# Performance work log

Measured on AMD Instinct MI355X. Metric: run time of the kernel, lower is better.

## Reference

```python
import jax, jax.numpy as jnp
import numpy as np

B, S, D, E, TOP_K = 2, 1024, 1024, 8, 2
H = 4 * D  # FFN hidden


def setup_inputs() -> dict:
    key = jax.random.key(0)
    ks = jax.random.split(key, 12)
    sc = 0.02
    return {
        "x": jax.random.normal(ks[0], (B, S, D), jnp.float32),
        # gate: nn.Linear(D, E) -> weight [E, D], bias [E]; routing bias param [E]
        "Wg": jax.random.normal(ks[1], (E, D), jnp.float32) * sc,
        "bg": jnp.zeros((E,), jnp.float32),
        "bias": jnp.zeros((E,), jnp.float32),
        # routed experts: stacked Linear(D,4D) and Linear(4D,D) weights (torch layout [out,in])
        "W1": jax.random.normal(ks[2], (E, H, D), jnp.float32) * sc,
        "b1": jnp.zeros((E, H), jnp.float32),
        "W2": jax.random.normal(ks[3], (E, D, H), jnp.float32) * sc,
        "b2": jnp.zeros((E, D), jnp.float32),
        # shared expert
        "Ws1": jax.random.normal(ks[4], (H, D), jnp.float32) * sc,
        "bs1": jnp.zeros((H,), jnp.float32),
        "Ws2": jax.random.normal(ks[5], (D, H), jnp.float32) * sc,
        "bs2": jnp.zeros((D,), jnp.float32),
    }


def reference(x, Wg, bg, bias, W1, b1, W2, b2, Ws1, bs1, Ws2, bs2):
    b, s, d = x.shape
    xf = x.reshape(-1, d)  # [T, D]
    T = xf.shape[0]

    # sigmoid gating with learnable routing bias
    scores = jax.nn.sigmoid(xf @ Wg.T + bg + bias)          # [T, E]
    top_scores, top_idx = jax.lax.top_k(scores, TOP_K)      # [T, K]

    # per-token per-expert combine weights (zero for unselected experts)
    weights = jnp.zeros((T, E), scores.dtype)
    weights = weights.at[jnp.arange(T)[:, None], top_idx].add(top_scores)  # [T, E]

    # dense grouped expert MLP (mask-and-matmul form of gather-GEMM-scatter)
    h = jax.nn.gelu(jnp.einsum("td,ehd->teh", xf, W1) + b1, approximate=False)  # [T, E, H]
    eo = jnp.einsum("teh,edh->ted", h, W2) + b2                                  # [T, E, D]
    combined = jnp.einsum("ted,te->td", eo, weights)                             # [T, D]

    # shared expert applied to every token
    shared = jax.nn.gelu(xf @ Ws1.T + bs1, approximate=False) @ Ws2.T + bs2      # [T, D]

    return (shared + combined).reshape(b, s, d)
```

## Files before the change

kernel.cpp:

```cpp
#include <hip/hip_runtime.h>
#include <hip/hip_bf16.h>
#include <math.h>

#define NTOK 2048
#define DDIM 1024
#define HDIM 4096
#define NEXP 8
#define NROWS (3 * NTOK)
#define KSPLIT2 2

typedef __bf16 bf16x8 __attribute__((ext_vector_type(8)));
typedef float f32x4 __attribute__((ext_vector_type(4)));
typedef __attribute__((address_space(1))) char as1_char;
typedef __attribute__((address_space(3))) char as3_char;

__device__ __forceinline__ void async16(const void* g, void* l) {
  __builtin_amdgcn_global_load_lds((as1_char*)g, (as3_char*)l, 16, 0, 0);
}

__device__ __forceinline__ float gelu_fast(float v) {
  const float x = v * 0.70710678118654752f;
  const float ax = fabsf(x);
  const float t = __builtin_amdgcn_rcpf(1.0f + 0.3275911f * ax);
  float p = 1.061405429f;
  p = p * t - 1.453152027f;
  p = p * t + 1.421413741f;
  p = p * t - 0.284496736f;
  p = p * t + 0.254829592f;
  const float y = 1.0f - p * t * __expf(-ax * ax);
  const float erfv = copysignf(y, x);
  return 0.5f * v * (1.0f + erfv);
}

__device__ __forceinline__ int off_of(const int* __restrict__ counts, int e) {
  if (e >= NEXP) return 2 * NTOK;
  int s = 0;
  for (int i = 0; i < e; ++i) s += counts[i];
  return s;
}

__device__ __forceinline__ void cvt2048(const float* __restrict__ src,
                                        __hip_bfloat16* __restrict__ dst,
                                        int tid) {
  const size_t i = (size_t)tid * 8;
  const float4 a = *(const float4*)(src + i);
  const float4 b = *(const float4*)(src + i + 4);
  union { __hip_bfloat16 h[8]; uint4 u; } p;
  p.h[0] = __float2bfloat16(a.x); p.h[1] = __float2bfloat16(a.y);
  p.h[2] = __float2bfloat16(a.z); p.h[3] = __float2bfloat16(a.w);
  p.h[4] = __float2bfloat16(b.x); p.h[5] = __float2bfloat16(b.y);
  p.h[6] = __float2bfloat16(b.z); p.h[7] = __float2bfloat16(b.w);
  *(uint4*)(dst + i) = p.u;
}

__global__ void __launch_bounds__(256) moe_pre(
    const float* __restrict__ x, const float* __restrict__ Wg,
    const float* __restrict__ bg, const float* __restrict__ bias,
    const float* __restrict__ W1, const float* __restrict__ Ws1,
    __hip_bfloat16* __restrict__ xbf, __hip_bfloat16* __restrict__ W1bf,
    __hip_bfloat16* __restrict__ Ws1bf, float* __restrict__ out,
    int* __restrict__ counts, int* __restrict__ topk_idx,
    float* __restrict__ topk_w, int* __restrict__ slot) {
  const int b = blockIdx.x, tid = threadIdx.x;
  if (b < 512) {
    const int t = b * 4 + (tid >> 6);
    const int lane = tid & 63;
    float xv[16];
#pragma unroll
    for (int q = 0; q < 16; ++q) xv[q] = x[(size_t)t * DDIM + q * 64 + lane];
    float sc[NEXP];
#pragma unroll
    for (int e = 0; e < NEXP; ++e) {
      float s = 0.f;
#pragma unroll
      for (int q = 0; q < 16; ++q) s += xv[q] * Wg[(size_t)e * DDIM + q * 64 + lane];
#pragma unroll
      for (int o = 32; o > 0; o >>= 1) s += __shfl_xor(s, o, 64);
      sc[e] = 1.0f / (1.0f + expf(-(s + bg[e] + bias[e])));
    }
    if (lane == 0) {
      int k0 = 0;
      for (int e = 1; e < NEXP; ++e)
        if (sc[e] > sc[k0]) k0 = e;
      int k1 = (k0 == 0) ? 1 : 0;
      for (int e = 0; e < NEXP; ++e) {
        if (e == k0) continue;
        if (sc[e] > sc[k1]) k1 = e;
      }
      topk_idx[t * 2 + 0] = k0;
      topk_idx[t * 2 + 1] = k1;
      topk_w[t * 2 + 0] = sc[k0];
      topk_w[t * 2 + 1] = sc[k1];
      slot[t * 2 + 0] = atomicAdd(&counts[k0], 1);
      slot[t * 2 + 1] = atomicAdd(&counts[k1], 1);
    }
    return;
  }
  const int cb = b - 512;
  if (cb < 1024) { cvt2048(x + (size_t)cb * 2048, xbf + (size_t)cb * 2048, tid); return; }
  if (cb < 17408) { const size_t o = (size_t)(cb - 1024) * 2048; cvt2048(W1 + o, W1bf + o, tid); return; }
  if (cb < 19456) { const size_t o = (size_t)(cb - 17408) * 2048; cvt2048(Ws1 + o, Ws1bf + o, tid); return; }
  const size_t o = (size_t)(cb - 19456) * 2048 + (size_t)tid * 8;
  *(float4*)(out + o) = make_float4(0.f, 0.f, 0.f, 0.f);
  *(float4*)(out + o + 4) = make_float4(0.f, 0.f, 0.f, 0.f);
}

__device__ __forceinline__ void gemm_core(const char* const ga[4], const char* const gb[4],
                                          char* sm, int Kbytes, int tid,
                                          f32x4 acc[4][4]) {
  const int w = tid >> 6, l = tid & 63;
  const int lr = l & 15, quad = l >> 4;
  const int wr = w >> 1, wc = w & 1;
  const int s8 = lr & 7;
  const int slot0 = (quad ^ s8) * 16;
  const int slot1 = ((4 + quad) ^ s8) * 16;
  const int abase = (wr * 64 + lr) * 128;
  const int bbase = 16384 + (wc * 64 + lr) * 128;
  const int niter = Kbytes >> 7;

  auto stage = [&](int it, int buf) {
    char* base = sm + buf * 32768;
    const int kb = it * 128;
#pragma unroll
    for (int q = 0; q < 4; ++q) {
      async16(ga[q] + kb, base + w * 4096 + q * 1024);
      async16(gb[q] + kb, base + 16384 + w * 4096 + q * 1024);
    }
  };

  stage(0, 0);
  for (int i = 0; i < niter; ++i) {
    const int cur = i & 1;
    if (i + 1 < niter) {
      stage(i + 1, cur ^ 1);
      __builtin_amdgcn_s_waitcnt(0x0F78);
    } else {
      __builtin_amdgcn_s_waitcnt(0x0F70);
    }
    __builtin_amdgcn_s_barrier();
    const char* rb = sm + cur * 32768;
    bf16x8 av[4][2], bv[4][2];
#pragma unroll
    for (int i2 = 0; i2 < 4; ++i2) {
      av[i2][0] = *(const bf16x8*)(rb + abase + i2 * 2048 + slot0);
      av[i2][1] = *(const bf16x8*)(rb + abase + i2 * 2048 + slot1);
    }
#pragma unroll
    for (int j = 0; j < 4; ++j) {
      bv[j][0] = *(const bf16x8*)(rb + bbase + j * 2048 + slot0);
      bv[j][1] = *(const bf16x8*)(rb + bbase + j * 2048 + slot1);
    }
#pragma unroll
    for (int s = 0; s < 2; ++s)
#pragma unroll
      for (int i2 = 0; i2 < 4; ++i2)
#pragma unroll
        for (int j = 0; j < 4; ++j)
          acc[i2][j] = __builtin_amdgcn_mfma_f32_16x16x32_bf16(av[i2][s], bv[j][s], acc[i2][j], 0, 0, 0);
    __builtin_amdgcn_s_barrier();
  }
}

__device__ __forceinline__ void gemm2_core(const char* const ga[4], const char* const gb[2],
                                           char* sm, int Kbytes, int tid,
                                           f32x4 acc[4][2]) {
  const int w = tid >> 6, l = tid & 63;
  const int lr = l & 15, quad = l >> 4;
  const int wr = w >> 1, wc = w & 1;
  const int s8 = lr & 7;
  const int slot0 = (quad ^ s8) * 16;
  const int slot1 = ((4 + quad) ^ s8) * 16;
  const int abase = (wr * 64 + lr) * 128;
  const int bbase = 16384 + (wc * 32 + lr) * 128;
  const int niter = Kbytes >> 7;

  auto stage = [&](int it, int buf) {
    char* base = sm + buf * 24576;
    const int kb = it * 128;
#pragma unroll
    for (int q = 0; q < 4; ++q)
      async16(ga[q] + kb, base + w * 4096 + q * 1024);
#pragma unroll
    for (int q = 0; q < 2; ++q)
      async16(gb[q] + kb, base + 16384 + w * 2048 + q * 1024);
  };

  stage(0, 0);
  for (int i = 0; i < niter; ++i) {
    const int cur = i & 1;
    if (i + 1 < niter) {
      stage(i + 1, cur ^ 1);
      __builtin_amdgcn_s_waitcnt(0x0F76);
    } else {
      __builtin_amdgcn_s_waitcnt(0x0F70);
    }
    __builtin_amdgcn_s_barrier();
    const char* rb = sm + cur * 24576;
    bf16x8 av[4][2], bv[2][2];
#pragma unroll
    for (int i2 = 0; i2 < 4; ++i2) {
      av[i2][0] = *(const bf16x8*)(rb + abase + i2 * 2048 + slot0);
      av[i2][1] = *(const bf16x8*)(rb + abase + i2 * 2048 + slot1);
    }
#pragma unroll
    for (int j = 0; j < 2; ++j) {
      bv[j][0] = *(const bf16x8*)(rb + bbase + j * 2048 + slot0);
      bv[j][1] = *(const bf16x8*)(rb + bbase + j * 2048 + slot1);
    }
#pragma unroll
    for (int s = 0; s < 2; ++s)
#pragma unroll
      for (int i2 = 0; i2 < 4; ++i2)
#pragma unroll
        for (int j = 0; j < 2; ++j)
          acc[i2][j] = __builtin_amdgcn_mfma_f32_16x16x32_bf16(av[i2][s], bv[j][s], acc[i2][j], 0, 0, 0);
    __builtin_amdgcn_s_barrier();
  }
}

__device__ __forceinline__ void xcd_decode(int hw, int& g, int& m) {
  m = (hw >> 3) & 7;
  g = (hw & 7) + 8 * (hw >> 6);
}

__global__ void moe_scatter(const int* __restrict__ counts,
                            const int* __restrict__ topk_idx, const float* __restrict__ topk_w,
                            const int* __restrict__ slot,
                            int* __restrict__ row_token, float* __restrict__ row_w) {
  const int t = blockIdx.x * blockDim.x + threadIdx.x;
  if (t >= NTOK) return;
#pragma unroll
  for (int k = 0; k < 2; ++k) {
    const int e = topk_idx[t * 2 + k];
    const int rg = off_of(counts, e) + slot[t * 2 + k];
    row_token[rg] = t;
    row_w[rg] = topk_w[t * 2 + k];
  }
  row_token[2 * NTOK + t] = t;
  row_w[2 * NTOK + t] = 1.0f;
}

__device__ __forceinline__ void cvt_w2_quota(int b, const float* __restrict__ W2,
                                             const float* __restrict__ Ws2,
                                             __hip_bfloat16* __restrict__ W2bf,
                                             __hip_bfloat16* __restrict__ Ws2bf,
                                             int tid) {
  const float* src;
  __hip_bfloat16* dst;
  size_t base;
  if (b < 4096) { src = W2; dst = W2bf; base = (size_t)b * 8192; }
  else          { src = Ws2; dst = Ws2bf; base = (size_t)(b - 4096) * 8192; }
#pragma unroll
  for (int k = 0; k < 8; ++k) {
    const size_t i = base + (size_t)k * 1024 + (size_t)tid * 4;
    const float4 a = *(const float4*)(src + i);
    union { __hip_bfloat16 h[4]; uint2 u; } p;
    p.h[0] = __float2bfloat16(a.x); p.h[1] = __float2bfloat16(a.y);
    p.h[2] = __float2bfloat16(a.z); p.h[3] = __float2bfloat16(a.w);
    *(uint2*)(dst + i) = p.u;
  }
}

__global__ void __launch_bounds__(256) moe_gemm1(
    const __hip_bfloat16* __restrict__ xbf, const __hip_bfloat16* __restrict__ W1bf,
    const float* __restrict__ b1, const __hip_bfloat16* __restrict__ Ws1bf,
    const float* __restrict__ bs1, const int* __restrict__ counts,
    const int* __restrict__ row_token,
    __hip_bfloat16* __restrict__ h1, const float* __restrict__ W2,
    const float* __restrict__ Ws2, __hip_bfloat16* __restrict__ W2bf,
    __hip_bfloat16* __restrict__ Ws2bf) {
  __shared__ alignas(16) char sm[65536];
  const int tid = threadIdx.x;
  int g, m;
  xcd_decode(blockIdx.x, g, m);
  const int nt = m + 8 * (g & 3);
  const int mt = (g >> 2) & 15;
  const int e = g >> 6;
  const int cnt = (e < NEXP) ? counts[e] : NTOK;
  if (mt * 128 >= cnt) {
    cvt_w2_quota(blockIdx.x, W2, Ws2, W2bf, Ws2bf, tid);
    return;
  }
  const int off = off_of(counts, e);
  const __hip_bfloat16* Bw = (e < NEXP) ? (W1bf + (size_t)e * HDIM * DDIM) : Ws1bf;
  const float* bb = (e < NEXP) ? (b1 + e * HDIM) : bs1;

  const int w = tid >> 6, l = tid & 63;
  const int rl8 = l >> 3;
  const int cg = ((l & 7) ^ rl8) * 16;

  const char* ga[4];
  const char* gb[4];
#pragma unroll
  for (int q = 0; q < 4; ++q) {
    const int r = mt * 128 + w * 32 + q * 8 + rl8;
    const int c = (r < cnt) ? r : (cnt - 1);
    const int tok = row_token[off + c];
    ga[q] = (const char*)xbf + (size_t)tok * (DDIM * 2) + cg;
    gb[q] = (const char*)Bw + (size_t)(nt * 128 + w * 32 + q * 8 + rl8) * (DDIM * 2) + cg;
  }

  f32x4 acc[4][4] = {};
  gemm_core(ga, gb, sm, DDIM * 2, tid, acc);

  const int lr = l & 15, quad = l >> 4, wr = w >> 1, wc = w & 1;
#pragma unroll
  for (int i = 0; i < 4; ++i) {
#pragma unroll
    for (int r = 0; r < 4; ++r) {
      const int rowe = mt * 128 + wr * 64 + i * 16 + quad * 4 + r;
      if (rowe >= cnt) continue;
      const size_t orow = (size_t)(off + rowe) * HDIM;
#pragma unroll
      for (int j = 0; j < 4; ++j) {
        const int h = nt * 128 + wc * 64 + j * 16 + lr;
        const float v = acc[i][j][r] + bb[h];
        h1[orow + h] = __float2bfloat16(gelu_fast(v));
      }
    }
  }
  cvt_w2_quota(blockIdx.x, W2, Ws2, W2bf, Ws2bf, tid);
}

__global__ void __launch_bounds__(256) moe_gemm2(
    const __hip_bfloat16* __restrict__ h1, const __hip_bfloat16* __restrict__ W2bf,
    const float* __restrict__ b2, const __hip_bfloat16* __restrict__ Ws2bf,
    const float* __restrict__ bs2, const int* __restrict__ counts,
    const int* __restrict__ row_token,
    const float* __restrict__ row_w, float* __restrict__ out) {
  __shared__ alignas(16) char sm[49152];
  int g, m;
  xcd_decode(blockIdx.x, g, m);
  const int nt = m + 8 * (g & 1);
  const int kc = (g >> 1) & 1;
  const int mt = (g >> 2) & 15;
  const int e = g >> 6;
  const int cnt = (e < NEXP) ? counts[e] : NTOK;
  if (mt * 128 >= cnt) return;
  const int off = off_of(counts, e);
  const __hip_bfloat16* Bw = (e < NEXP) ? (W2bf + (size_t)e * DDIM * HDIM) : Ws2bf;
  const float* bb = (e < NEXP) ? (b2 + e * DDIM) : bs2;

  const int tid = threadIdx.x;
  const int w = tid >> 6, l = tid & 63;
  const int rl8 = l >> 3;
  const int cg = ((l & 7) ^ rl8) * 16;
  const int KB = (HDIM * 2) / KSPLIT2;
  const size_t kofs = (size_t)kc * KB;

  const char* ga[4];
  const char* gb[2];
#pragma unroll
  for (int q = 0; q < 4; ++q) {
    const int ar = mt * 128 + w * 32 + q * 8 + rl8;
    ga[q] = (const char*)h1 + (size_t)(off + ar) * (HDIM * 2) + kofs + cg;
  }
#pragma unroll
  for (int q = 0; q < 2; ++q) {
    const int br = nt * 64 + w * 16 + q * 8 + rl8;
    gb[q] = (const char*)Bw + (size_t)br * (HDIM * 2) + kofs + cg;
  }

  f32x4 acc[4][2] = {};
  gemm2_core(ga, gb, sm, KB, tid, acc);

  const int lr = l & 15, quad = l >> 4, wr = w >> 1, wc = w & 1;
#pragma unroll
  for (int i = 0; i < 4; ++i) {
#pragma unroll
    for (int r = 0; r < 4; ++r) {
      const int rowe = mt * 128 + wr * 64 + i * 16 + quad * 4 + r;
      if (rowe >= cnt) continue;
      const int rg = off + rowe;
      const int tok = row_token[rg];
      const float wt = row_w[rg];
#pragma unroll
      for (int j = 0; j < 2; ++j) {
        const int d = nt * 64 + wc * 32 + j * 16 + lr;
        const float base = (kc == 0) ? bb[d] : 0.f;
        atomicAdd(&out[(size_t)tok * DDIM + d], wt * (acc[i][j][r] + base));
      }
    }
  }
}

extern "C" void kernel_launch(void* const* d_in, const int* in_sizes, int n_in,
                              void* d_out, int out_size, void* d_ws, size_t ws_size,
                              hipStream_t stream) {
  (void)in_sizes; (void)n_in; (void)out_size; (void)ws_size;
  const float* x    = (const float*)d_in[0];
  const float* Wg   = (const float*)d_in[1];
  const float* bg   = (const float*)d_in[2];
  const float* bias = (const float*)d_in[3];
  const float* W1   = (const float*)d_in[4];
  const float* b1   = (const float*)d_in[5];
  const float* W2   = (const float*)d_in[6];
  const float* b2   = (const float*)d_in[7];
  const float* Ws1  = (const float*)d_in[8];
  const float* bs1  = (const float*)d_in[9];
  const float* Ws2  = (const float*)d_in[10];
  const float* bs2  = (const float*)d_in[11];
  float* out = (float*)d_out;

  char* ws = (char*)d_ws;
  size_t cur = 0;
  auto take = [&](size_t b) -> void* {
    void* p = ws + cur;
    cur += (b + 255) & ~(size_t)255;
    return p;
  };
  int* counts    = (int*)take(NEXP * 4);
  int* topk_idx  = (int*)take(NTOK * 2 * 4);
  float* topk_w  = (float*)take(NTOK * 2 * 4);
  int* slot      = (int*)take(NTOK * 2 * 4);
  int* row_token = (int*)take(NROWS * 4);
  float* row_w   = (float*)take(NROWS * 4);
  __hip_bfloat16* xbf   = (__hip_bfloat16*)take((size_t)NTOK * DDIM * 2);
  __hip_bfloat16* W1bf  = (__hip_bfloat16*)take((size_t)NEXP * HDIM * DDIM * 2);
  __hip_bfloat16* W2bf  = (__hip_bfloat16*)take((size_t)NEXP * DDIM * HDIM * 2);
  __hip_bfloat16* Ws1bf = (__hip_bfloat16*)take((size_t)HDIM * DDIM * 2);
  __hip_bfloat16* Ws2bf = (__hip_bfloat16*)take((size_t)DDIM * HDIM * 2);
  __hip_bfloat16* h1    = (__hip_bfloat16*)take((size_t)(NROWS + 64) * HDIM * 2);

  hipMemsetAsync(counts, 0, NEXP * sizeof(int), stream);

  moe_pre<<<20992, 256, 0, stream>>>(x, Wg, bg, bias, W1, Ws1,
                                     xbf, W1bf, Ws1bf, out,
                                     counts, topk_idx, topk_w, slot);

  moe_scatter<<<NTOK / 256, 256, 0, stream>>>(counts, topk_idx, topk_w, slot,
                                              row_token, row_w);

  moe_gemm1<<<4608, 256, 0, stream>>>(xbf, W1bf, b1, Ws1bf, bs1, counts,
                                      row_token, h1, W2, Ws2, W2bf, Ws2bf);

  moe_gemm2<<<4608, 256, 0, stream>>>(h1, W2bf, b2, Ws2bf, bs2, counts,
                                      row_token, row_w, out);
}
```

Measured before the change: 314.2 us.

## Double wavefronts per block in both expert GEMMs, shrinking per-wave tiles

Result: faster. 296.8 us (median of 2 runs) (-5.5%).

```diff
diff --git a/kernel.cpp b/kernel.cpp
--- a/kernel.cpp
+++ b/kernel.cpp
@@ -105,26 +105,26 @@
   *(float4*)(out + o + 4) = make_float4(0.f, 0.f, 0.f, 0.f);
 }
 
-__device__ __forceinline__ void gemm_core(const char* const ga[4], const char* const gb[4],
+__device__ __forceinline__ void gemm_core(const char* const ga[2], const char* const gb[2],
                                           char* sm, int Kbytes, int tid,
-                                          f32x4 acc[4][4]) {
+                                          f32x4 acc[4][2]) {
   const int w = tid >> 6, l = tid & 63;
   const int lr = l & 15, quad = l >> 4;
-  const int wr = w >> 1, wc = w & 1;
+  const int wm = w >> 2, wn = w & 3;
   const int s8 = lr & 7;
   const int slot0 = (quad ^ s8) * 16;
   const int slot1 = ((4 + quad) ^ s8) * 16;
-  const int abase = (wr * 64 + lr) * 128;
-  const int bbase = 16384 + (wc * 64 + lr) * 128;
+  const int abase = (wm * 64 + lr) * 128;
+  const int bbase = 16384 + (wn * 32 + lr) * 128;
   const int niter = Kbytes >> 7;
 
   auto stage = [&](int it, int buf) {
     char* base = sm + buf * 32768;
     const int kb = it * 128;
 #pragma unroll
-    for (int q = 0; q < 4; ++q) {
-      async16(ga[q] + kb, base + w * 4096 + q * 1024);
-      async16(gb[q] + kb, base + 16384 + w * 4096 + q * 1024);
+    for (int q = 0; q < 2; ++q) {
+      async16(ga[q] + kb, base + w * 2048 + q * 1024);
+      async16(gb[q] + kb, base + 16384 + w * 2048 + q * 1024);
     }
   };
 
@@ -133,20 +133,20 @@
     const int cur = i & 1;
     if (i + 1 < niter) {
       stage(i + 1, cur ^ 1);
-      __builtin_amdgcn_s_waitcnt(0x0F78);
+      __builtin_amdgcn_s_waitcnt(0x0F74);
     } else {
       __builtin_amdgcn_s_waitcnt(0x0F70);
     }
     __builtin_amdgcn_s_barrier();
     const char* rb = sm + cur * 32768;
-    bf16x8 av[4][2], bv[4][2];
+    bf16x8 av[4][2], bv[2][2];
 #pragma unroll
     for (int i2 = 0; i2 < 4; ++i2) {
       av[i2][0] = *(const bf16x8*)(rb + abase + i2 * 2048 + slot0);
       av[i2][1] = *(const bf16x8*)(rb + abase + i2 * 2048 + slot1);
     }
 #pragma unroll
-    for (int j = 0; j < 4; ++j) {
+    for (int j = 0; j < 2; ++j) {
       bv[j][0] = *(const bf16x8*)(rb + bbase + j * 2048 + slot0);
       bv[j][1] = *(const bf16x8*)(rb + bbase + j * 2048 + slot1);
     }
@@ -155,34 +155,31 @@
 #pragma unroll
       for (int i2 = 0; i2 < 4; ++i2)
 #pragma unroll
-        for (int j = 0; j < 4; ++j)
+        for (int j = 0; j < 2; ++j)
           acc[i2][j] = __builtin_amdgcn_mfma_f32_16x16x32_bf16(av[i2][s], bv[j][s], acc[i2][j], 0, 0, 0);
     __builtin_amdgcn_s_barrier();
   }
 }
 
-__device__ __forceinline__ void gemm2_core(const char* const ga[4], const char* const gb[2],
+__device__ __forceinline__ void gemm2_core(const char* const ga[2], const char* gb0,
                                            char* sm, int Kbytes, int tid,
-                                           f32x4 acc[4][2]) {
+                                           f32x4 acc[2][2]) {
   const int w = tid >> 6, l = tid & 63;
   const int lr = l & 15, quad = l >> 4;
-  const int wr = w >> 1, wc = w & 1;
+  const int wm = w >> 1, wn = w & 1;
   const int s8 = lr & 7;
   const int slot0 = (quad ^ s8) * 16;
   const int slot1 = ((4 + quad) ^ s8) * 16;
-  const int abase = (wr * 64 + lr) * 128;
-  const int bbase = 16384 + (wc * 32 + lr) * 128;
+  const int abase = (wm * 32 + lr) * 128;
+  const int bbase = 16384 + (wn * 32 + lr) * 128;
   const int niter = Kbytes >> 7;
 
   auto stage = [&](int it, int buf) {
     char* base = sm + buf * 24576;
     const int kb = it * 128;
-#pragma unroll
-    for (int q = 0; q < 4; ++q)
-      async16(ga[q] + kb, base + w * 4096 + q * 1024);
-#pragma unroll
-    for (int q = 0; q < 2; ++q)
-      async16(gb[q] + kb, base + 16384 + w * 2048 + q * 1024);
+    async16(ga[0] + kb, base + w * 2048);
+    async16(ga[1] + kb, base + w * 2048 + 1024);
+    async16(gb0 + kb, base + 16384 + w * 1024);
   };
 
   stage(0, 0);
@@ -190,15 +187,15 @@
     const int cur = i & 1;
     if (i + 1 < niter) {
       stage(i + 1, cur ^ 1);
-      __builtin_amdgcn_s_waitcnt(0x0F76);
+      __builtin_amdgcn_s_waitcnt(0x0F73);
     } else {
       __builtin_amdgcn_s_waitcnt(0x0F70);
     }
     __builtin_amdgcn_s_barrier();
     const char* rb = sm + cur * 24576;
-    bf16x8 av[4][2], bv[2][2];
-#pragma unroll
-    for (int i2 = 0; i2 < 4; ++i2) {
+    bf16x8 av[2][2], bv[2][2];
+#pragma unroll
+    for (int i2 = 0; i2 < 2; ++i2) {
       av[i2][0] = *(const bf16x8*)(rb + abase + i2 * 2048 + slot0);
       av[i2][1] = *(const bf16x8*)(rb + abase + i2 * 2048 + slot1);
     }
@@ -210,7 +207,7 @@
 #pragma unroll
     for (int s = 0; s < 2; ++s)
 #pragma unroll
-      for (int i2 = 0; i2 < 4; ++i2)
+      for (int i2 = 0; i2 < 2; ++i2)
 #pragma unroll
         for (int j = 0; j < 2; ++j)
           acc[i2][j] = __builtin_amdgcn_mfma_f32_16x16x32_bf16(av[i2][s], bv[j][s], acc[i2][j], 0, 0, 0);
@@ -251,8 +248,8 @@
   if (b < 4096) { src = W2; dst = W2bf; base = (size_t)b * 8192; }
   else          { src = Ws2; dst = Ws2bf; base = (size_t)(b - 4096) * 8192; }
 #pragma unroll
-  for (int k = 0; k < 8; ++k) {
-    const size_t i = base + (size_t)k * 1024 + (size_t)tid * 4;
+  for (int k = 0; k < 4; ++k) {
+    const size_t i = base + (size_t)k * 2048 + (size_t)tid * 4;
     const float4 a = *(const float4*)(src + i);
     union { __hip_bfloat16 h[4]; uint2 u; } p;
     p.h[0] = __float2bfloat16(a.x); p.h[1] = __float2bfloat16(a.y);
@@ -261,7 +258,7 @@
   }
 }
 
-__global__ void __launch_bounds__(256) moe_gemm1(
+__global__ void __launch_bounds__(512, 4) moe_gemm1(
     const __hip_bfloat16* __restrict__ xbf, const __hip_bfloat16* __restrict__ W1bf,
     const float* __restrict__ b1, const __hip_bfloat16* __restrict__ Ws1bf,
     const float* __restrict__ bs1, const int* __restrict__ counts,
@@ -289,31 +286,31 @@
   const int rl8 = l >> 3;
   const int cg = ((l & 7) ^ rl8) * 16;
 
-  const char* ga[4];
-  const char* gb[4];
-#pragma unroll
-  for (int q = 0; q < 4; ++q) {
-    const int r = mt * 128 + w * 32 + q * 8 + rl8;
+  const char* ga[2];
+  const char* gb[2];
+#pragma unroll
+  for (int q = 0; q < 2; ++q) {
+    const int r = mt * 128 + (2 * w + q) * 8 + rl8;
     const int c = (r < cnt) ? r : (cnt - 1);
     const int tok = row_token[off + c];
     ga[q] = (const char*)xbf + (size_t)tok * (DDIM * 2) + cg;
-    gb[q] = (const char*)Bw + (size_t)(nt * 128 + w * 32 + q * 8 + rl8) * (DDIM * 2) + cg;
-  }
-
-  f32x4 acc[4][4] = {};
+    gb[q] = (const char*)Bw + (size_t)(nt * 128 + (2 * w + q) * 8 + rl8) * (DDIM * 2) + cg;
+  }
+
+  f32x4 acc[4][2] = {};
   gemm_core(ga, gb, sm, DDIM * 2, tid, acc);
 
-  const int lr = l & 15, quad = l >> 4, wr = w >> 1, wc = w & 1;
+  const int lr = l & 15, quad = l >> 4, wm = w >> 2, wn = w & 3;
 #pragma unroll
   for (int i = 0; i < 4; ++i) {
 #pragma unroll
     for (int r = 0; r < 4; ++r) {
-      const int rowe = mt * 128 + wr * 64 + i * 16 + quad * 4 + r;
+      const int rowe = mt * 128 + wm * 64 + i * 16 + quad * 4 + r;
       if (rowe >= cnt) continue;
       const size_t orow = (size_t)(off + rowe) * HDIM;
 #pragma unroll
-      for (int j = 0; j < 4; ++j) {
-        const int h = nt * 128 + wc * 64 + j * 16 + lr;
+      for (int j = 0; j < 2; ++j) {
+        const int h = nt * 128 + wn * 32 + j * 16 + lr;
         const float v = acc[i][j][r] + bb[h];
         h1[orow + h] = __float2bfloat16(gelu_fast(v));
       }
@@ -322,7 +319,7 @@
   cvt_w2_quota(blockIdx.x, W2, Ws2, W2bf, Ws2bf, tid);
 }
 
-__global__ void __launch_bounds__(256) moe_gemm2(
+__global__ void __launch_bounds__(512, 6) moe_gemm2(
     const __hip_bfloat16* __restrict__ h1, const __hip_bfloat16* __restrict__ W2bf,
     const float* __restrict__ b2, const __hip_bfloat16* __restrict__ Ws2bf,
     const float* __restrict__ bs2, const int* __restrict__ counts,
@@ -348,35 +345,31 @@
   const int KB = (HDIM * 2) / KSPLIT2;
   const size_t kofs = (size_t)kc * KB;
 
-  const char* ga[4];
-  const char* gb[2];
-#pragma unroll
-  for (int q = 0; q < 4; ++q) {
-    const int ar = mt * 128 + w * 32 + q * 8 + rl8;
+  const char* ga[2];
+#pragma unroll
+  for (int q = 0; q < 2; ++q) {
+    const int ar = mt * 128 + (2 * w + q) * 8 + rl8;
     ga[q] = (const char*)h1 + (size_t)(off + ar) * (HDIM * 2) + kofs + cg;
   }
-#pragma unroll
-  for (int q = 0; q < 2; ++q) {
-    const int br = nt * 64 + w * 16 + q * 8 + rl8;
-    gb[q] = (const char*)Bw + (size_t)br * (HDIM * 2) + kofs + cg;
-  }
-
-  f32x4 acc[4][2] = {};
-  gemm2_core(ga, gb, sm, KB, tid, acc);
-
-  const int lr = l & 15, quad = l >> 4, wr = w >> 1, wc = w & 1;
-#pragma unroll
-  for (int i = 0; i < 4; ++i) {
+  const char* gb0 = (const char*)Bw +
+      (size_t)(nt * 64 + w * 8 + rl8) * (HDIM * 2) + kofs + cg;
+
+  f32x4 acc[2][2] = {};
+  gemm2_core(ga, gb0, sm, KB, tid, acc);
+
+  const int lr = l & 15, quad = l >> 4, wm = w >> 1, wn = w & 1;
+#pragma unroll
+  for (int i = 0; i < 2; ++i) {
 #pragma unroll
     for (int r = 0; r < 4; ++r) {
-      const int rowe = mt * 128 + wr * 64 + i * 16 + quad * 4 + r;
+      const int rowe = mt * 128 + wm * 32 + i * 16 + quad * 4 + r;
       if (rowe >= cnt) continue;
       const int rg = off + rowe;
       const int tok = row_token[rg];
       const float wt = row_w[rg];
 #pragma unroll
       for (int j = 0; j < 2; ++j) {
-        const int d = nt * 64 + wc * 32 + j * 16 + lr;
+        const int d = nt * 64 + wn * 32 + j * 16 + lr;
         const float base = (kc == 0) ? bb[d] : 0.f;
         atomicAdd(&out[(size_t)tok * DDIM + d], wt * (acc[i][j][r] + base));
       }
@@ -431,9 +424,9 @@
   moe_scatter<<<NTOK / 256, 256, 0, stream>>>(counts, topk_idx, topk_w, slot,
                                               row_token, row_w);
 
-  moe_gemm1<<<4608, 256, 0, stream>>>(xbf, W1bf, b1, Ws1bf, bs1, counts,
+  moe_gemm1<<<4608, 512, 0, stream>>>(xbf, W1bf, b1, Ws1bf, bs1, counts,
                                       row_token, h1, W2, Ws2, W2bf, Ws2bf);
 
-  moe_gemm2<<<4608, 256, 0, stream>>>(h1, W2bf, b2, Ws2bf, bs2, counts,
+  moe_gemm2<<<4608, 512, 0, stream>>>(h1, W2bf, b2, Ws2bf, bs2, counts,
                                       row_token, row_w, out);
 }
```
